# Kernel tuning notes

Hardware: AMD Instinct MI355X
Metric: run time of the kernel (lower is better)

The kernel has to match this reference:

```python
import jax, jax.numpy as jnp
import numpy as np

B, S, D = 8, 2048, 1024
NEG = -1000000000.0  # float32 masking constant from original code


def setup_inputs() -> dict:
    key = jax.random.key(0)
    kq, kk, kv, km = jax.random.split(key, 4)
    q = jax.random.normal(kq, (B, S, D), dtype=jnp.float32)
    k = jax.random.normal(kk, (B, S, D), dtype=jnp.float32)
    v = jax.random.normal(kv, (B, S, D), dtype=jnp.float32)
    mask = (jax.random.uniform(km, (B, 1, S)) < 0.1).astype(jnp.float32)
    return {"q": q, "k": k, "v": v, "mask": mask}


def reference(q, k, v, mask):
    scale = jnp.asarray(D ** -0.5, dtype=q.dtype)
    # [B,S,S] = q @ k^T, scaled
    logits = jnp.einsum("bqd,bkd->bqk", q, k) * scale
    logits = logits + mask * NEG  # mask broadcasts over query axis
    attn = jax.nn.softmax(logits, axis=-1)
    return jnp.einsum("bqk,bkd->bqd", attn, v)
```

## Files before the change

### kernel.cpp

```cpp
#include <hip/hip_runtime.h>
#include <hip/hip_bf16.h>

#define NB 8
#define SS 2048
#define DDIM 1024

typedef __attribute__((ext_vector_type(8))) short bf16x8;
typedef __attribute__((ext_vector_type(4))) float f32x4;

__device__ inline void gload_lds16(const void* g, void* l) {
  __builtin_amdgcn_global_load_lds(
      (const __attribute__((address_space(1))) void*)g,
      (__attribute__((address_space(3))) void*)l, 16, 0, 0);
}

__device__ inline ushort f2bf(float f) {
  union { float f; unsigned int u; } v;
  v.f = f;
  unsigned int u = v.u;
  unsigned int r = (u + 0x7FFFu + ((u >> 16) & 1u)) >> 16;
  return (ushort)r;
}

__device__ inline unsigned int pack2(float a, float b) {
  return (unsigned int)f2bf(a) | ((unsigned int)f2bf(b) << 16);
}

__global__ void init_zero(float* __restrict__ p, int n) {
  int i = blockIdx.x * 256 + threadIdx.x;
  if (i < n) p[i] = 0.f;
}

__global__ void conv_bf16(const float* __restrict__ in, ushort* __restrict__ out,
                          int n8) {
  int i = blockIdx.x * 256 + threadIdx.x;
  if (i >= n8) return;
  const float4* p = (const float4*)in + (size_t)i * 2;
  float4 a = p[0], b = p[1];
  uint4 o;
  o.x = pack2(a.x, a.y);
  o.y = pack2(a.z, a.w);
  o.z = pack2(b.x, b.y);
  o.w = pack2(b.z, b.w);
  ((uint4*)out)[i] = o;
}

__global__ void conv_transpose_v(const float* __restrict__ V,
                                 ushort* __restrict__ VT) {
  __shared__ ushort tile[64][65];
  const int b = blockIdx.z;
  const int k0 = blockIdx.x * 64;
  const int d0 = blockIdx.y * 64;
  const float* Vb = V + (size_t)b * SS * DDIM;
  ushort* VTb = VT + (size_t)b * DDIM * SS;
  const int t = threadIdx.x;
#pragma unroll
  for (int i = 0; i < 16; i++) {
    int flat = i * 256 + t;
    int r = flat >> 6, c = flat & 63;
    tile[r][c] = f2bf(Vb[(size_t)(k0 + r) * DDIM + d0 + c]);
  }
  __syncthreads();
#pragma unroll
  for (int i = 0; i < 16; i++) {
    int flat = i * 256 + t;
    int r = flat >> 6, c = flat & 63;
    VTb[(size_t)(d0 + r) * SS + k0 + c] = tile[c][r];
  }
}

#define MFMA16(mh, nh)                                                        \
  _Pragma("unroll") for (int ks = 0; ks < 2; ks++)                            \
  _Pragma("unroll") for (int mi = 0; mi < 4; mi++)                            \
  _Pragma("unroll") for (int ni = 0; ni < 2; ni++)                            \
      acc[mh][mi][nh][ni] = __builtin_amdgcn_mfma_f32_16x16x32_bf16(          \
          af[mi][ks], bf[ni][ks], acc[mh][mi][nh][ni], 0, 0, 0);

#define PHASE(mh, nh)                                                         \
  __builtin_amdgcn_s_barrier();                                               \
  asm volatile("s_waitcnt lgkmcnt(0)" ::: "memory");                          \
  __builtin_amdgcn_sched_barrier(0);                                          \
  __builtin_amdgcn_s_setprio(1);                                              \
  MFMA16(mh, nh);                                                             \
  __builtin_amdgcn_s_setprio(0);                                              \
  __builtin_amdgcn_sched_barrier(0);

#define VMW(n) asm volatile("s_waitcnt vmcnt(" #n ")" ::: "memory")
#define ENDP() __builtin_amdgcn_s_barrier()

#define RD_A(d, h)                                                            \
  _Pragma("unroll") for (int mi = 0; mi < 4; mi++) {                          \
    const char* _p = ldsc + (d) * 65536 + (h) * 16384 + aoff[mi];             \
    af[mi][0] = *(const bf16x8*)(_p + koff0);                                 \
    af[mi][1] = *(const bf16x8*)(_p + koff1);                                 \
  }

#define RD_B(d, h)                                                            \
  _Pragma("unroll") for (int ni = 0; ni < 2; ni++) {                          \
    const char* _p = ldsc + (d) * 65536 + 32768 + (h) * 16384 + boff[ni];     \
    bf[ni][0] = *(const bf16x8*)(_p + koff0);                                 \
    bf[ni][1] = *(const bf16x8*)(_p + koff1);                                 \
  }

#define STAGE(dbuf, isB, h, kt_)                                              \
  do {                                                                        \
    const ushort* _s = (isB) ? Bb : Ab;                                       \
    const int _t0 = (isB) ? tileN : tileM;                                    \
    char* _lb = ldsc + (dbuf) * 65536 + (isB) * 32768 + (h) * 16384;          \
    gload_lds16(_s + (size_t)(_t0 + (h) * 128 + r0) * K + (kt_) * 64 + c8,    \
                _lb + ol0);                                                   \
    gload_lds16(_s + (size_t)(_t0 + (h) * 128 + r1) * K + (kt_) * 64 + c8,    \
                _lb + ol1);                                                   \
  } while (0)

template <bool EXPEPI, typename OutT>
__global__ __launch_bounds__(512, 2) void gemm_bt(
    const ushort* __restrict__ A, const ushort* __restrict__ Bm,
    OutT* __restrict__ C, const float* __restrict__ maskp,
    float* __restrict__ rowsum, int M, int N, int K, float alpha) {
  __shared__ __attribute__((aligned(128))) char ldsc[131072];
  const int tid = threadIdx.x;
  const int wave = tid >> 6, lane = tid & 63;
  const int quad = lane >> 4, l16 = lane & 15;
  const int wm = wave >> 2, wn = wave & 3;

  const int gx = gridDim.x, gy = gridDim.y;
  const int lin = blockIdx.x + gx * (blockIdx.y + gy * blockIdx.z);
  const int nwg = gx * gy * (int)gridDim.z;
  const int cpx = nwg >> 3;
  const int swz = (lin & 7) * cpx + (lin >> 3);
  const int bz = swz / (gx * gy);
  const int rem = swz - bz * (gx * gy);
  const int by = rem / gx;
  const int bx = rem - by * gx;

  const int b = bz;
  const ushort* Ab = A + (size_t)b * M * K;
  const ushort* Bb = Bm + (size_t)b * N * K;
  const int tileM = by * 256, tileN = bx * 256;

  const int ol0 = wave * 2048 + lane * 16;
  const int ol1 = ol0 + 1024;
  const int r0 = ol0 >> 7;
  const int r1 = r0 + 8;
  const int c8 = (((lane & 7) ^ (r0 & 7)) * 8);

  const int x7 = lane & 7;
  const int koff0 = ((quad) ^ x7) * 16;
  const int koff1 = ((4 + quad) ^ x7) * 16;
  int aoff[4], boff[2];
#pragma unroll
  for (int mi = 0; mi < 4; mi++) aoff[mi] = (wm * 64 + mi * 16 + l16) * 128;
#pragma unroll
  for (int ni = 0; ni < 2; ni++) boff[ni] = (wn * 32 + ni * 16 + l16) * 128;

  f32x4 acc[2][4][2][2];
#pragma unroll
  for (int mh = 0; mh < 2; mh++)
#pragma unroll
    for (int mi = 0; mi < 4; mi++)
#pragma unroll
      for (int nh = 0; nh < 2; nh++)
#pragma unroll
        for (int ni = 0; ni < 2; ni++)
          acc[mh][mi][nh][ni] = (f32x4){0.f, 0.f, 0.f, 0.f};

  bf16x8 af[4][2], bf[2][2];
  const int NKT = K >> 6;

  STAGE(0, 0, 0, 0);
  STAGE(0, 1, 0, 0);
  STAGE(0, 1, 1, 0);
  STAGE(0, 0, 1, 0);
  VMW(4);
  __builtin_amdgcn_s_barrier();

  for (int kt = 0; kt < NKT - 1; ++kt) {
    const int d = kt & 1, dn = d ^ 1;
    RD_A(d, 0); RD_B(d, 0); STAGE(dn, 0, 0, kt + 1);
    PHASE(0, 0); VMW(4); ENDP();
    RD_B(d, 1);             STAGE(dn, 1, 0, kt + 1);
    PHASE(0, 1); VMW(4); ENDP();
    RD_A(d, 1);             STAGE(dn, 1, 1, kt + 1);
    PHASE(1, 1); ENDP();
    RD_B(d, 0);             STAGE(dn, 0, 1, kt + 1);
    PHASE(1, 0); VMW(4); ENDP();
  }
  {
    const int d = (NKT - 1) & 1;
    RD_A(d, 0); RD_B(d, 0);
    PHASE(0, 0); VMW(2); ENDP();
    RD_B(d, 1);
    PHASE(0, 1); VMW(0); ENDP();
    RD_A(d, 1);
    PHASE(1, 1); ENDP();
    RD_B(d, 0);
    PHASE(1, 0); ENDP();
  }

  OutT* Cb = C + (size_t)b * M * N;
  if (EXPEPI) {
    const float* mb = maskp + (size_t)b * N;
    float mv[2][2];
#pragma unroll
    for (int nh = 0; nh < 2; nh++)
#pragma unroll
      for (int ni = 0; ni < 2; ni++)
        mv[nh][ni] = mb[tileN + nh * 128 + wn * 32 + ni * 16 + l16] * (-1e9f);
#pragma unroll
    for (int mh = 0; mh < 2; mh++)
#pragma unroll
    for (int mi = 0; mi < 4; mi++) {
#pragma unroll
      for (int rr = 0; rr < 4; rr++) {
        const int row = tileM + mh * 128 + wm * 64 + mi * 16 + quad * 4 + rr;
        float s = 0.f;
#pragma unroll
        for (int nh = 0; nh < 2; nh++)
#pragma unroll
        for (int ni = 0; ni < 2; ni++) {
          const int col = tileN + nh * 128 + wn * 32 + ni * 16 + l16;
          float e = __expf(acc[mh][mi][nh][ni][rr] * alpha + mv[nh][ni]);
          ((ushort*)Cb)[(size_t)row * N + col] = f2bf(e);
          s += e;
        }
        s += __shfl_xor(s, 1, 64);
        s += __shfl_xor(s, 2, 64);
        s += __shfl_xor(s, 4, 64);
        s += __shfl_xor(s, 8, 64);
        if (l16 == 0) atomicAdd(&rowsum[(size_t)b * M + row], s);
      }
    }
  } else {
#pragma unroll
    for (int mh = 0; mh < 2; mh++)
#pragma unroll
    for (int mi = 0; mi < 4; mi++) {
      float inv[4];
#pragma unroll
      for (int rr = 0; rr < 4; rr++) {
        const int row = tileM + mh * 128 + wm * 64 + mi * 16 + quad * 4 + rr;
        inv[rr] = 1.0f / rowsum[(size_t)b * M + row];
      }
#pragma unroll
      for (int nh = 0; nh < 2; nh++)
#pragma unroll
      for (int ni = 0; ni < 2; ni++) {
        const int col = tileN + nh * 128 + wn * 32 + ni * 16 + l16;
#pragma unroll
        for (int rr = 0; rr < 4; rr++) {
          const int row = tileM + mh * 128 + wm * 64 + mi * 16 + quad * 4 + rr;
          ((float*)Cb)[(size_t)row * N + col] =
              acc[mh][mi][nh][ni][rr] * alpha * inv[rr];
        }
      }
    }
  }
}

extern "C" void kernel_launch(void* const* d_in, const int* in_sizes, int n_in,
                              void* d_out, int out_size, void* d_ws, size_t ws_size,
                              hipStream_t stream) {
  const float* q = (const float*)d_in[0];
  const float* k = (const float*)d_in[1];
  const float* v = (const float*)d_in[2];
  const float* mask = (const float*)d_in[3];
  float* out = (float*)d_out;

  const size_t pQ = (size_t)SS * DDIM * 2;
  const size_t pP = (size_t)SS * SS * 2;
  const size_t pR = (size_t)SS * 4;

  int gb = 8;
  while (gb > 1 && (size_t)gb * (3 * pQ + pP + pR) > ws_size) gb >>= 1;

  for (int b0 = 0; b0 < NB; b0 += gb) {
    char* w = (char*)d_ws;
    ushort* qb = (ushort*)w;
    ushort* kb = (ushort*)(w + (size_t)gb * pQ);
    ushort* vtb = (ushort*)(w + (size_t)gb * pQ * 2);
    ushort* Sc = (ushort*)(w + (size_t)gb * pQ * 3);
    float* rowsum = (float*)(w + (size_t)gb * (pQ * 3 + pP));

    const float* qg = q + (size_t)b0 * SS * DDIM;
    const float* kg = k + (size_t)b0 * SS * DDIM;
    const float* vg = v + (size_t)b0 * SS * DDIM;
    const float* mg = mask + (size_t)b0 * SS;
    float* og = out + (size_t)b0 * SS * DDIM;

    const int nrs = gb * SS;
    init_zero<<<(nrs + 255) / 256, 256, 0, stream>>>(rowsum, nrs);
    const int n8 = gb * SS * DDIM / 8;
    conv_bf16<<<n8 / 256, 256, 0, stream>>>(qg, qb, n8);
    conv_bf16<<<n8 / 256, 256, 0, stream>>>(kg, kb, n8);
    conv_transpose_v<<<dim3(SS / 64, DDIM / 64, gb), 256, 0, stream>>>(vg, vtb);
    gemm_bt<true, ushort><<<dim3(SS / 256, SS / 256, gb), 512, 0, stream>>>(
        qb, kb, Sc, mg, rowsum, SS, SS, DDIM, 0.03125f);
    gemm_bt<false, float><<<dim3(DDIM / 256, SS / 256, gb), 512, 0, stream>>>(
        Sc, vtb, og, nullptr, rowsum, SS, DDIM, SS, 1.0f);
  }
}
```

Before: 368.4 us.

## Deepen GEMM prefetch pipeline, double-buffer B fragments, vectorize V transpose

The GEMM main loop is restructured to process two k-tiles per iteration. It prefetches further ahead (seven stage loads in flight initially) and keeps two B-fragment register sets, so B fragments no longer have to be re-read from LDS for the final phase. It also relaxes the LDS wait to lgkmcnt(8) after issuing loads. Separately, the V convert-transpose kernel now uses float4 loads and 16-byte stores instead of scalar accesses. The extra register sets and deeper prefetch raise register pressure, and the new wait counts must match the number of in-flight operations exactly.

Result: slower. 389.6 us (+5.7%).

```diff
diff --git a/kernel.cpp b/kernel.cpp
--- a/kernel.cpp
+++ b/kernel.cpp
@@ -55,37 +55,45 @@
   ushort* VTb = VT + (size_t)b * DDIM * SS;
   const int t = threadIdx.x;
 #pragma unroll
-  for (int i = 0; i < 16; i++) {
-    int flat = i * 256 + t;
-    int r = flat >> 6, c = flat & 63;
-    tile[r][c] = f2bf(Vb[(size_t)(k0 + r) * DDIM + d0 + c]);
+  for (int i = 0; i < 4; i++) {
+    int j = i * 256 + t;
+    int r = j >> 4, cg = j & 15;
+    float4 f = *(const float4*)(Vb + (size_t)(k0 + r) * DDIM + d0 + cg * 4);
+    tile[r][cg * 4 + 0] = f2bf(f.x);
+    tile[r][cg * 4 + 1] = f2bf(f.y);
+    tile[r][cg * 4 + 2] = f2bf(f.z);
+    tile[r][cg * 4 + 3] = f2bf(f.w);
   }
   __syncthreads();
 #pragma unroll
-  for (int i = 0; i < 16; i++) {
-    int flat = i * 256 + t;
-    int r = flat >> 6, c = flat & 63;
-    VTb[(size_t)(d0 + r) * SS + k0 + c] = tile[c][r];
-  }
-}
-
-#define MFMA16(mh, nh)                                                        \
+  for (int i = 0; i < 2; i++) {
+    int j = i * 256 + t;
+    int r = j >> 3, cg = j & 7;
+    ushort u[8];
+#pragma unroll
+    for (int u8 = 0; u8 < 8; u8++) u[u8] = tile[cg * 8 + u8][r];
+    *(uint4*)(VTb + (size_t)(d0 + r) * SS + k0 + cg * 8) = *(uint4*)u;
+  }
+}
+
+#define MFMA16(mh, nh, BF)                                                    \
   _Pragma("unroll") for (int ks = 0; ks < 2; ks++)                            \
   _Pragma("unroll") for (int mi = 0; mi < 4; mi++)                            \
   _Pragma("unroll") for (int ni = 0; ni < 2; ni++)                            \
       acc[mh][mi][nh][ni] = __builtin_amdgcn_mfma_f32_16x16x32_bf16(          \
-          af[mi][ks], bf[ni][ks], acc[mh][mi][nh][ni], 0, 0, 0);
-
-#define PHASE(mh, nh)                                                         \
+          af[mi][ks], BF[ni][ks], acc[mh][mi][nh][ni], 0, 0, 0);
+
+#define PHASE(mh, nh, BF)                                                     \
   __builtin_amdgcn_s_barrier();                                               \
   asm volatile("s_waitcnt lgkmcnt(0)" ::: "memory");                          \
   __builtin_amdgcn_sched_barrier(0);                                          \
   __builtin_amdgcn_s_setprio(1);                                              \
-  MFMA16(mh, nh);                                                             \
+  MFMA16(mh, nh, BF);                                                         \
   __builtin_amdgcn_s_setprio(0);                                              \
   __builtin_amdgcn_sched_barrier(0);
 
 #define VMW(n) asm volatile("s_waitcnt vmcnt(" #n ")" ::: "memory")
+#define LGK8 asm volatile("s_waitcnt lgkmcnt(8)" ::: "memory")
 #define ENDP() __builtin_amdgcn_s_barrier()
 
 #define RD_A(d, h)                                                            \
@@ -95,11 +103,11 @@
     af[mi][1] = *(const bf16x8*)(_p + koff1);                                 \
   }
 
-#define RD_B(d, h)                                                            \
+#define RD_B(d, h, dst)                                                       \
   _Pragma("unroll") for (int ni = 0; ni < 2; ni++) {                          \
     const char* _p = ldsc + (d) * 65536 + 32768 + (h) * 16384 + boff[ni];     \
-    bf[ni][0] = *(const bf16x8*)(_p + koff0);                                 \
-    bf[ni][1] = *(const bf16x8*)(_p + koff1);                                 \
+    dst[ni][0] = *(const bf16x8*)(_p + koff0);                                \
+    dst[ni][1] = *(const bf16x8*)(_p + koff1);                                \
   }
 
 #define STAGE(dbuf, isB, h, kt_)                                              \
@@ -165,37 +173,54 @@
         for (int ni = 0; ni < 2; ni++)
           acc[mh][mi][nh][ni] = (f32x4){0.f, 0.f, 0.f, 0.f};
 
-  bf16x8 af[4][2], bf[2][2];
+  bf16x8 af[4][2], bfa[2][2], bfb[2][2];
   const int NKT = K >> 6;
+  const int NIT = NKT >> 1;
 
   STAGE(0, 0, 0, 0);
   STAGE(0, 1, 0, 0);
   STAGE(0, 1, 1, 0);
   STAGE(0, 0, 1, 0);
-  VMW(4);
+  STAGE(1, 0, 0, 1);
+  STAGE(1, 1, 0, 1);
+  STAGE(1, 1, 1, 1);
+  VMW(6);
   __builtin_amdgcn_s_barrier();
 
-  for (int kt = 0; kt < NKT - 1; ++kt) {
-    const int d = kt & 1, dn = d ^ 1;
-    RD_A(d, 0); RD_B(d, 0); STAGE(dn, 0, 0, kt + 1);
-    PHASE(0, 0); VMW(4); ENDP();
-    RD_B(d, 1);             STAGE(dn, 1, 0, kt + 1);
-    PHASE(0, 1); VMW(4); ENDP();
-    RD_A(d, 1);             STAGE(dn, 1, 1, kt + 1);
-    PHASE(1, 1); ENDP();
-    RD_B(d, 0);             STAGE(dn, 0, 1, kt + 1);
-    PHASE(1, 0); VMW(4); ENDP();
+  for (int it = 0; it < NIT - 1; ++it) {
+    const int tb = 2 * it;
+    RD_A(0, 0); RD_B(0, 0, bfa); STAGE(1, 0, 1, tb + 1); LGK8;
+    PHASE(0, 0, bfa); ENDP();
+    RD_B(0, 1, bfb); STAGE(0, 0, 0, tb + 2);
+    PHASE(0, 1, bfb); ENDP();
+    RD_A(0, 1); STAGE(0, 1, 0, tb + 2);
+    PHASE(1, 1, bfb); ENDP();
+    STAGE(0, 1, 1, tb + 2);
+    PHASE(1, 0, bfa); VMW(6); ENDP();
+    RD_A(1, 0); RD_B(1, 0, bfa); STAGE(0, 0, 1, tb + 2); LGK8;
+    PHASE(0, 0, bfa); ENDP();
+    RD_B(1, 1, bfb); STAGE(1, 0, 0, tb + 3);
+    PHASE(0, 1, bfb); ENDP();
+    RD_A(1, 1); STAGE(1, 1, 0, tb + 3);
+    PHASE(1, 1, bfb); ENDP();
+    STAGE(1, 1, 1, tb + 3);
+    PHASE(1, 0, bfa); VMW(6); ENDP();
   }
   {
-    const int d = (NKT - 1) & 1;
-    RD_A(d, 0); RD_B(d, 0);
-    PHASE(0, 0); VMW(2); ENDP();
-    RD_B(d, 1);
-    PHASE(0, 1); VMW(0); ENDP();
-    RD_A(d, 1);
-    PHASE(1, 1); ENDP();
-    RD_B(d, 0);
-    PHASE(1, 0); ENDP();
+    RD_A(0, 0); RD_B(0, 0, bfa); STAGE(1, 0, 1, NKT - 1); LGK8;
+    PHASE(0, 0, bfa); ENDP();
+    RD_B(0, 1, bfb);
+    PHASE(0, 1, bfb); ENDP();
+    RD_A(0, 1);
+    PHASE(1, 1, bfb); ENDP();
+    PHASE(1, 0, bfa); VMW(0); ENDP();
+    RD_A(1, 0); RD_B(1, 0, bfa);
+    PHASE(0, 0, bfa); ENDP();
+    RD_B(1, 1, bfb);
+    PHASE(0, 1, bfb); ENDP();
+    RD_A(1, 1);
+    PHASE(1, 1, bfb); ENDP();
+    PHASE(1, 0, bfa);
   }
 
   OutT* Cb = C + (size_t)b * M * N;
```

## Fuse zero-init, Q/K bf16 conversion and V transpose into one prep kernel

Applied to the files above, without the earlier changes.

Replaces four preprocessing launches (rowsum zeroing, Q and K bf16 conversion, V convert-transpose) with a single tiled prep kernel. The V transpose now reads float4 vectors and writes 16-byte packed bf16 stores instead of scalar 2-byte accesses. The aim is to cut launch overhead and improve memory coalescing in the bandwidth-bound conversion stage. In exchange, each block does more mixed work, and the LDS column reads in the transpose may hit more bank conflicts.

After: 368.8 us. About the same (+0.1%).

```diff
diff --git a/kernel.cpp b/kernel.cpp
--- a/kernel.cpp
+++ b/kernel.cpp
@@ -26,46 +26,64 @@
   return (unsigned int)f2bf(a) | ((unsigned int)f2bf(b) << 16);
 }
 
-__global__ void init_zero(float* __restrict__ p, int n) {
-  int i = blockIdx.x * 256 + threadIdx.x;
-  if (i < n) p[i] = 0.f;
-}
-
-__global__ void conv_bf16(const float* __restrict__ in, ushort* __restrict__ out,
-                          int n8) {
-  int i = blockIdx.x * 256 + threadIdx.x;
-  if (i >= n8) return;
-  const float4* p = (const float4*)in + (size_t)i * 2;
-  float4 a = p[0], b = p[1];
-  uint4 o;
-  o.x = pack2(a.x, a.y);
-  o.y = pack2(a.z, a.w);
-  o.z = pack2(b.x, b.y);
-  o.w = pack2(b.z, b.w);
-  ((uint4*)out)[i] = o;
-}
-
-__global__ void conv_transpose_v(const float* __restrict__ V,
-                                 ushort* __restrict__ VT) {
+__global__ void prep(const float* __restrict__ q, const float* __restrict__ k,
+                     const float* __restrict__ v, ushort* __restrict__ qb,
+                     ushort* __restrict__ kb, ushort* __restrict__ vtb,
+                     float* __restrict__ rowsum) {
   __shared__ ushort tile[64][65];
   const int b = blockIdx.z;
-  const int k0 = blockIdx.x * 64;
+  const int s0 = blockIdx.x * 64;
   const int d0 = blockIdx.y * 64;
-  const float* Vb = V + (size_t)b * SS * DDIM;
-  ushort* VTb = VT + (size_t)b * DDIM * SS;
   const int t = threadIdx.x;
-#pragma unroll
-  for (int i = 0; i < 16; i++) {
-    int flat = i * 256 + t;
-    int r = flat >> 6, c = flat & 63;
-    tile[r][c] = f2bf(Vb[(size_t)(k0 + r) * DDIM + d0 + c]);
+  const size_t base = (size_t)b * SS * DDIM;
+
+  if (blockIdx.x == 0 && blockIdx.y == 0) {
+#pragma unroll
+    for (int j = 0; j < SS / 256; j++)
+      rowsum[(size_t)b * SS + j * 256 + t] = 0.f;
+  }
+
+#pragma unroll
+  for (int pass = 0; pass < 2; pass++) {
+    const float* in = (pass ? k : q) + base;
+    ushort* out = (pass ? kb : qb) + base;
+#pragma unroll
+    for (int i = 0; i < 2; i++) {
+      int j = i * 256 + t;
+      int r = j >> 3, cg = j & 7;
+      const float* p = in + (size_t)(s0 + r) * DDIM + d0 + cg * 8;
+      float4 a = *(const float4*)p;
+      float4 c = *(const float4*)(p + 4);
+      uint4 o;
+      o.x = pack2(a.x, a.y);
+      o.y = pack2(a.z, a.w);
+      o.z = pack2(c.x, c.y);
+      o.w = pack2(c.z, c.w);
+      *(uint4*)(out + (size_t)(s0 + r) * DDIM + d0 + cg * 8) = o;
+    }
+  }
+
+  const float* Vb = v + base;
+  ushort* VTb = vtb + (size_t)b * DDIM * SS;
+#pragma unroll
+  for (int i = 0; i < 4; i++) {
+    int j = i * 256 + t;
+    int r = j >> 4, cg = j & 15;
+    float4 f = *(const float4*)(Vb + (size_t)(s0 + r) * DDIM + d0 + cg * 4);
+    tile[r][cg * 4 + 0] = f2bf(f.x);
+    tile[r][cg * 4 + 1] = f2bf(f.y);
+    tile[r][cg * 4 + 2] = f2bf(f.z);
+    tile[r][cg * 4 + 3] = f2bf(f.w);
   }
   __syncthreads();
 #pragma unroll
-  for (int i = 0; i < 16; i++) {
-    int flat = i * 256 + t;
-    int r = flat >> 6, c = flat & 63;
-    VTb[(size_t)(d0 + r) * SS + k0 + c] = tile[c][r];
+  for (int i = 0; i < 2; i++) {
+    int j = i * 256 + t;
+    int r = j >> 3, cg = j & 7;
+    ushort u[8];
+#pragma unroll
+    for (int u8 = 0; u8 < 8; u8++) u[u8] = tile[cg * 8 + u8][r];
+    *(uint4*)(VTb + (size_t)(d0 + r) * SS + s0 + cg * 8) = *(uint4*)u;
   }
 }
 
@@ -288,12 +306,8 @@
     const float* mg = mask + (size_t)b0 * SS;
     float* og = out + (size_t)b0 * SS * DDIM;
 
-    const int nrs = gb * SS;
-    init_zero<<<(nrs + 255) / 256, 256, 0, stream>>>(rowsum, nrs);
-    const int n8 = gb * SS * DDIM / 8;
-    conv_bf16<<<n8 / 256, 256, 0, stream>>>(qg, qb, n8);
-    conv_bf16<<<n8 / 256, 256, 0, stream>>>(kg, kb, n8);
-    conv_transpose_v<<<dim3(SS / 64, DDIM / 64, gb), 256, 0, stream>>>(vg, vtb);
+    prep<<<dim3(SS / 64, DDIM / 64, gb), 256, 0, stream>>>(qg, kg, vg, qb, kb,
+                                                           vtb, rowsum);
     gemm_bt<true, ushort><<<dim3(SS / 256, SS / 256, gb), 512, 0, stream>>>(
         qb, kb, Sc, mg, rowsum, SS, SS, DDIM, 0.03125f);
     gemm_bt<false, float><<<dim3(DDIM / 256, SS / 256, gb), 512, 0, stream>>>(
```
